# Optimization experiments

Hardware: AMD Instinct MI355X
Metric: run time of the kernel (lower is better)

## Reference

```python
import jax, jax.numpy as jnp
import numpy as np

S = 8          # conv_size == octree branching factor
EMBED = 512    # transformer embed_dim
HEAD = 64      # head_dim
NV = 3         # num_vocab (1=empty, 2=mixed, 3=full; 0=padding)
T2 = 8192      # latent tokens T''
LEN1 = T2 * S          # penultimate-layer tokens (65536)
MIX = LEN1 // 4        # number of mixed tokens in penultimate layer
LEN0 = MIX * S         # last-layer tokens (131072)


def _gelu(x):
    return jax.nn.gelu(x, approximate=False)  # torch nn.GELU default (erf)


def _block_conv(x, W, b):
    # BlockConvolution: within each non-overlapping block of S tokens, output
    # offset j has its own kernel over block inputs 0..j (block-causal).
    # x: [T, Cin], W: [S(offset j), Cout, Cin, S(tap i)], b: [S, Cout]
    xb = x.reshape(-1, S, x.shape[-1])                      # [K, S, Cin]
    Wm = W * jnp.tril(jnp.ones((S, S), W.dtype))[:, None, None, :]
    out = jnp.einsum('kic,joci->kjo', xb, Wm) + b[None]
    return out.reshape(-1, W.shape[1])


def _conv(x, W, b):
    # Conv1d kernel=stride=S. x: [T, Cin], W: [Cout, Cin, S] -> [T//S, Cout]
    xb = x.reshape(-1, S, x.shape[-1])
    return jnp.einsum('kic,oci->ko', xb, W) + b


def _deconv(x, W, b):
    # ConvTranspose1d kernel=stride=S. x: [T, Cin], W: [Cin, Cout, S] -> [T*S, Cout]
    out = jnp.einsum('kc,coj->kjo', x, W) + b
    return out.reshape(-1, W.shape[1])


def _pw(x, W, b):
    # pointwise Conv1d(k=1) / nn.Linear. W: [Cout, Cin]
    return x @ W.T + b


def _forward(value, x, emb_table, Wdc, bdc, bc0a_W, bc0a_b, bc0b_W, bc0b_b,
             bc1a_W, bc1a_b, bc1b_W, bc1b_b, Wd1, bd1, Wp1, bp1,
             Wd0, bd0, Wp0, bp0, Wl1, bl1, Wl2, bl2):
    v = value[0]
    val_1 = v[:LEN1]          # penultimate layer values
    val_0 = v[-LEN0:]         # last layer values (depth == max_depth)
    emb_0 = emb_table[val_0]                               # [LEN0, H]
    down = _conv(emb_0, Wdc, bdc)                          # down_convolution -> [MIX, H]
    idx = jnp.nonzero(val_1 == 2, size=MIX, fill_value=0)[0]  # mixed-token positions
    emb_1 = jnp.zeros((LEN1, HEAD), x.dtype).at[idx].set(down)
    # convolution_0: BC, GELU, BC   (applied to emb_0[:, :mix_1*8] == full emb_0)
    e0 = _block_conv(emb_0, bc0a_W, bc0a_b)
    e0 = _block_conv(_gelu(e0), bc0b_W, bc0b_b)
    # convolution_1: GELU, BC, GELU, BC
    e1 = _block_conv(_gelu(emb_1), bc1a_W, bc1a_b)
    e1 = _block_conv(_gelu(e1), bc1b_W, bc1b_b)
    # deconvolution_1: GELU, Deconv(E->H, S), GELU, Conv(k=1)
    y1 = _deconv(_gelu(x[0]), Wd1, bd1)                    # [LEN1, H]
    y1 = _pw(_gelu(y1), Wp1, bp1) + e1
    x0 = y1[idx]                                           # gather mixed rows -> [MIX, H]
    # deconvolution_0: GELU, Deconv(H->H, 8), GELU, Conv(k=1)
    y0 = _deconv(_gelu(x0), Wd0, bd0)                      # [LEN0, H]
    y0 = _pw(_gelu(y0), Wp0, bp0) + e0
    # linear: GELU, Linear(H,H), GELU, Linear(H, num_vocab)
    return _pw(_gelu(_pw(_gelu(y0), Wl1, bl1)), Wl2, bl2)[None]  # [1, LEN0, NV]


def setup_inputs():
    key = jax.random.key(0)
    ks = jax.random.split(key, 28)
    p = lambda k, sh: jax.random.normal(k, sh, jnp.float32) * 0.02
    # penultimate layer: values in {1,3}, every 4th token is mixed (==2)
    v1 = 1 + 2 * jax.random.bernoulli(ks[0], 0.5, (LEN1,)).astype(jnp.int32)
    v1 = v1.at[::4].set(2)
    v0 = jax.random.randint(ks[1], (LEN0,), 1, NV + 1, dtype=jnp.int32)
    value = jnp.concatenate([v1, v0])[None]
    depth = jnp.concatenate([jnp.full((LEN1,), 5, jnp.int32),
                             jnp.full((LEN0,), 6, jnp.int32)])[None]
    pos = jax.random.randint(ks[2], (1, LEN1 + LEN0, 3), 0, 64, dtype=jnp.int32)
    return dict(
        x=jax.random.normal(ks[3], (1, T2, EMBED), jnp.float32),
        value=value, depth=depth, pos=pos,
        emb_table=p(ks[4], (NV + 1, HEAD)).at[0].set(0.0),  # padding_idx=0
        Wdc=p(ks[5], (HEAD, HEAD, S)), bdc=p(ks[6], (HEAD,)),
        bc0a_W=p(ks[7], (S, HEAD, HEAD, S)), bc0a_b=p(ks[8], (S, HEAD)),
        bc0b_W=p(ks[9], (S, HEAD, HEAD, S)), bc0b_b=p(ks[10], (S, HEAD)),
        bc1a_W=p(ks[11], (S, HEAD, HEAD, S)), bc1a_b=p(ks[12], (S, HEAD)),
        bc1b_W=p(ks[13], (S, HEAD, HEAD, S)), bc1b_b=p(ks[14], (S, HEAD)),
        Wd1=p(ks[15], (EMBED, HEAD, S)), bd1=p(ks[16], (HEAD,)),
        Wp1=p(ks[17], (HEAD, HEAD)), bp1=p(ks[18], (HEAD,)),
        Wd0=p(ks[19], (HEAD, HEAD, S)), bd0=p(ks[20], (HEAD,)),
        Wp0=p(ks[21], (HEAD, HEAD)), bp0=p(ks[22], (HEAD,)),
        Wl1=p(ks[23], (HEAD, HEAD)), bl1=p(ks[24], (HEAD,)),
        Wl2=p(ks[25], (NV, HEAD)), bl2=p(ks[26], (NV,)),
    )


def reference(x, value, depth, pos, emb_table, Wdc, bdc, bc0a_W, bc0a_b, bc0b_W, bc0b_b,
              bc1a_W, bc1a_b, bc1b_W, bc1b_b, Wd1, bd1, Wp1, bp1, Wd0, bd0, Wp0, bp0,
              Wl1, bl1, Wl2, bl2):
    del depth, pos  # only used for length bookkeeping in the original; spatial_encoding is None
    return _forward(value, x, emb_table, Wdc, bdc, bc0a_W, bc0a_b, bc0b_W, bc0b_b,
                    bc1a_W, bc1a_b, bc1b_W, bc1b_b, Wd1, bd1, Wp1, bp1,
                    Wd0, bd0, Wp0, bp0, Wl1, bl1, Wl2, bl2)
```

## Files before the change

kernel.cpp:

```cpp
#include <hip/hip_runtime.h>
#include <hip/hip_bf16.h>
#include <cstddef>
#include <cstdint>

#define LEN1 65536
#define MIX  16384
#define LEN0 131072

typedef __hip_bfloat16 bf16;
typedef __attribute__((ext_vector_type(8))) short bfrag;
typedef __attribute__((ext_vector_type(4))) float ffrag;

__device__ __forceinline__ float gelu(float x){
    return 0.5f * x * (1.0f + erff(x * 0.70710678118654752440f));
}
__device__ __forceinline__ unsigned short f2bf_bits(float f){
    bf16 h = __float2bfloat16(f);
    return __builtin_bit_cast(unsigned short, h);
}
__device__ __forceinline__ float bfbits2f(unsigned short u){
    union { unsigned int i; float f; } v; v.i = ((unsigned int)u) << 16; return v.f;
}

__device__ __forceinline__ void gld_lds16(const void* g, void* l){
    __builtin_amdgcn_global_load_lds(
        (const __attribute__((address_space(1))) unsigned int*)g,
        (__attribute__((address_space(3))) unsigned int*)l, 16, 0, 0);
}


__global__ void k_zero4(float4* p){
    p[(size_t)blockIdx.x * 256 + threadIdx.x] = make_float4(0.f, 0.f, 0.f, 0.f);
}

__global__ void k_gelu_bf(const float4* __restrict__ in, ushort* __restrict__ out){
    size_t t = (size_t)blockIdx.x * 256 + threadIdx.x;
    float4 v = in[t];
    ushort4 o;
    o.x = f2bf_bits(gelu(v.x)); o.y = f2bf_bits(gelu(v.y));
    o.z = f2bf_bits(gelu(v.z)); o.w = f2bf_bits(gelu(v.w));
    *reinterpret_cast<ushort4*>(out + 4*t) = o;
}


__global__ void k_count(const int* __restrict__ val1, int* __restrict__ bcount){
    __shared__ int cnt;
    if (threadIdx.x == 0) cnt = 0;
    __syncthreads();
    int p = blockIdx.x * 256 + threadIdx.x;
    int m = (val1[p] == 2) ? 1 : 0;
    unsigned long long b = __ballot(m);
    if ((threadIdx.x & 63) == 0) atomicAdd(&cnt, __popcll(b));
    __syncthreads();
    if (threadIdx.x == 0) bcount[blockIdx.x] = cnt;
}

__global__ void k_scan(const int* __restrict__ bcount, int* __restrict__ bscan){
    __shared__ int s[256];
    int t = threadIdx.x;
    s[t] = bcount[t];
    __syncthreads();
    for (int off = 1; off < 256; off <<= 1){
        int v = (t >= off) ? s[t - off] : 0;
        __syncthreads();
        s[t] += v;
        __syncthreads();
    }
    bscan[t] = s[t] - bcount[t];
}

__global__ void k_write_idx(const int* __restrict__ val1, const int* __restrict__ bscan,
                            int* __restrict__ idx){
    __shared__ int loc[256];
    int t = threadIdx.x;
    int p = blockIdx.x * 256 + t;
    int m = (val1[p] == 2) ? 1 : 0;
    loc[t] = m;
    __syncthreads();
    for (int off = 1; off < 256; off <<= 1){
        int v = (t >= off) ? loc[t - off] : 0;
        __syncthreads();
        loc[t] += v;
        __syncthreads();
    }
    if (m){
        int g = bscan[blockIdx.x] + loc[t] - 1;
        if (g < MIX) idx[g] = p;
    }
}


__global__ void k_prep_PQ(const float* __restrict__ table, const float* __restrict__ Wdc,
                          const float* __restrict__ W0a, float* __restrict__ P,
                          float* __restrict__ Q){
    int tid = blockIdx.x * 256 + threadIdx.x;
    if (tid < 2048){
        int v = tid >> 9, i = (tid >> 6) & 7, o = tid & 63;
        float s = 0.f;
        for (int c = 0; c < 64; ++c) s += table[v*64 + c] * Wdc[(o*64 + c)*8 + i];
        P[tid] = s;
    } else if (tid < 2048 + 16384){
        int e = tid - 2048;
        int v = e >> 12, j = (e >> 9) & 7, i = (e >> 6) & 7, o = e & 63;
        float s = 0.f;
        for (int c = 0; c < 64; ++c) s += table[v*64 + c] * W0a[((j*64 + o)*64 + c)*8 + i];
        Q[e] = s;
    }
}

__global__ void k_prep_W(const float* __restrict__ W0b, const float* __restrict__ W1a,
                         const float* __restrict__ W1b, const float* __restrict__ Wd1,
                         const float* __restrict__ Wd0, const float* __restrict__ Wp1,
                         const float* __restrict__ Wp0, const float* __restrict__ Wl1,
                         ushort* __restrict__ BT0b, ushort* __restrict__ BT1a,
                         ushort* __restrict__ BT1b, ushort* __restrict__ BTd1,
                         ushort* __restrict__ BTd0, ushort* __restrict__ Wp1bf,
                         ushort* __restrict__ Wp0bf, ushort* __restrict__ Wl1p){
    int e = blockIdx.x * 256 + threadIdx.x;
    if (e < 786432){
        int m = e / 262144, r = e % 262144;
        int n = r >> 9, kk = r & 511;
        int j = n >> 6, o = n & 63;
        int i = kk >> 6, c = kk & 63;
        const float* W = (m == 0) ? W0b : ((m == 1) ? W1a : W1b);
        float v = (i <= j) ? W[((j*64 + o)*64 + c)*8 + i] : 0.0f;
        ((m == 0) ? BT0b : ((m == 1) ? BT1a : BT1b))[r] = f2bf_bits(v);
    } else if (e < 1048576){
        int r = e - 786432;
        int n = r >> 9, kk = r & 511;
        int j = n >> 6, o = n & 63;
        BTd1[r] = f2bf_bits(Wd1[(kk*64 + o)*8 + j]);
    } else if (e < 1081344){
        int r = e - 1048576;
        int n = r >> 6, c = r & 63;
        int j = n >> 6, o = n & 63;
        BTd0[r] = f2bf_bits(Wd0[(c*64 + o)*8 + j]);
    } else if (e < 1085440){
        int r = e - 1081344; Wp1bf[r] = f2bf_bits(Wp1[r]);
    } else if (e < 1089536){
        int r = e - 1085440; Wp0bf[r] = f2bf_bits(Wp0[r]);
    } else if (e < 1093632){
        int r = e - 1089536;
        int o2 = r >> 6, kcol = r & 63;
        int kf = kcol >> 5, q = (kcol >> 3) & 3, ee = kcol & 7;
        int o = kf*32 + ((ee < 4) ? (4*q + ee) : (16 + 4*q + ee - 4));
        Wl1p[r] = f2bf_bits(Wl1[o2*64 + o]);
    }
}


__global__ void k_down_scatter(const int* __restrict__ val0, const float* __restrict__ P,
                               const float* __restrict__ bdc, const int* __restrict__ idx,
                               ushort* __restrict__ gemb1){
    int t = blockIdx.x * 256 + threadIdx.x;
    int k = t >> 6, o = t & 63;
    float s = bdc[o];
    #pragma unroll
    for (int i = 0; i < 8; ++i){
        int v = val0[k*8 + i];
        s += P[(v*8 + i)*64 + o];
    }
    gemb1[(size_t)idx[k]*64 + o] = f2bf_bits(gelu(s));
}

__global__ void k_e0a(const int* __restrict__ val0, const float* __restrict__ Q,
                      const float* __restrict__ b0a, ushort* __restrict__ ge0a){
    int t = blockIdx.x * 256 + threadIdx.x;
    int k = t >> 6, o = t & 63;
    int v[8];
    #pragma unroll
    for (int i = 0; i < 8; ++i) v[i] = val0[k*8 + i];
    float acc[8];
    #pragma unroll
    for (int j = 0; j < 8; ++j) acc[j] = b0a[j*64 + o];
    #pragma unroll
    for (int i = 0; i < 8; ++i){
        const float* Qi = Q + v[i]*4096 + i*64 + o;
        #pragma unroll
        for (int j = i; j < 8; ++j) acc[j] += Qi[j*512];
    }
    #pragma unroll
    for (int j = 0; j < 8; ++j)
        ge0a[(size_t)k*512 + j*64 + o] = f2bf_bits(gelu(acc[j]));
}

template<int BM, int GATHER>
__device__ __forceinline__ void gemm_body(
    const ushort* __restrict__ A, const ushort* __restrict__ BT,
    const float* __restrict__ bias, int bmask,
    ushort* __restrict__ out, int N, int K, const int* __restrict__ idxmap,
    int gelu_flag, ushort* Atile, ushort* Btile, int rowBase, int colBase){
    constexpr int MI = BM / 32;
    const int tid  = threadIdx.x;
    const int lane = tid & 63;
    const int wv   = tid >> 6;
    const int wm   = wv >> 1, wn = wv & 1;

    ffrag acc[MI][4];
    #pragma unroll
    for (int mi = 0; mi < MI; ++mi)
        #pragma unroll
        for (int ni = 0; ni < 4; ++ni)
            #pragma unroll
            for (int r = 0; r < 4; ++r) acc[mi][ni][r] = 0.f;

    constexpr int ACH = BM * 4 / 256;
    int ar[ACH]; int as[ACH]; size_t arow[ACH];
    #pragma unroll
    for (int q = 0; q < ACH; ++q){
        int c = q*256 + tid;
        ar[q] = c >> 2; as[q] = (c & 3) ^ ((ar[q] >> 1) & 3);
        arow[q] = GATHER ? (size_t)idxmap[rowBase + ar[q]] : (size_t)(rowBase + ar[q]);
    }
    int b0c = tid, b1c = 256 + tid;
    int br0 = b0c >> 2, bs0 = (b0c & 3) ^ ((br0 >> 1) & 3);
    int br1 = b1c >> 2, bs1 = (b1c & 3) ^ ((br1 >> 1) & 3);

    for (int kt = 0; kt < K; kt += 32){
        #pragma unroll
        for (int q = 0; q < ACH; ++q)
            gld_lds16(A + arow[q]*K + kt + as[q]*8, (char*)Atile + (q*256 + tid)*16);
        gld_lds16(BT + (size_t)(colBase + br0)*K + kt + bs0*8, (char*)Btile + b0c*16);
        gld_lds16(BT + (size_t)(colBase + br1)*K + kt + bs1*8, (char*)Btile + b1c*16);
        __syncthreads();
        bfrag af[MI], bf[4];
        #pragma unroll
        for (int mi = 0; mi < MI; ++mi){
            int r = wm*(BM/2) + mi*16 + (lane & 15);
            int slot = (lane >> 4) ^ ((r >> 1) & 3);
            af[mi] = *reinterpret_cast<const bfrag*>((const char*)Atile + r*64 + slot*16);
        }
        #pragma unroll
        for (int ni = 0; ni < 4; ++ni){
            int r = wn*64 + ni*16 + (lane & 15);
            int slot = (lane >> 4) ^ ((r >> 1) & 3);
            bf[ni] = *reinterpret_cast<const bfrag*>((const char*)Btile + r*64 + slot*16);
        }
        #pragma unroll
        for (int mi = 0; mi < MI; ++mi)
            #pragma unroll
            for (int ni = 0; ni < 4; ++ni)
                acc[mi][ni] = __builtin_amdgcn_mfma_f32_16x16x32_bf16(af[mi], bf[ni], acc[mi][ni], 0, 0, 0);
        __syncthreads();
    }

    #pragma unroll
    for (int mi = 0; mi < MI; ++mi){
        #pragma unroll
        for (int ni = 0; ni < 4; ++ni){
            int col = colBase + wn*64 + ni*16 + (lane & 15);
            float bv = bias[col & bmask];
            #pragma unroll
            for (int r = 0; r < 4; ++r){
                size_t row = (size_t)rowBase + wm*(BM/2) + mi*16 + (lane >> 4)*4 + r;
                float v = acc[mi][ni][r] + bv;
                if (gelu_flag) v = gelu(v);
                out[row*N + col] = f2bf_bits(v);
            }
        }
    }
}

template<int BM, int GATHER>
__global__ __launch_bounds__(256) void k_mfma_gemm(
    const ushort* __restrict__ A, const ushort* __restrict__ BT,
    const float* __restrict__ bias, int bmask,
    ushort* __restrict__ out, int N, int K, const int* __restrict__ idxmap,
    int gelu_flag){
    __shared__ ushort Atile[BM*32];
    __shared__ ushort Btile[128*32];
    gemm_body<BM, GATHER>(A, BT, bias, bmask, out, N, K, idxmap, gelu_flag,
                          Atile, Btile, blockIdx.y * BM, blockIdx.x * 128);
}

__global__ __launch_bounds__(256) void k_gemm3(
    const ushort* __restrict__ A0, const ushort* __restrict__ A1, const ushort* __restrict__ A2,
    const ushort* __restrict__ B0, const ushort* __restrict__ B1, const ushort* __restrict__ B2,
    const float* __restrict__ bias0, const float* __restrict__ bias1, const float* __restrict__ bias2,
    int bm0, int bm1, int bm2,
    ushort* __restrict__ o0, ushort* __restrict__ o1, ushort* __restrict__ o2,
    int g0, int g1, int g2){
    int b = blockIdx.x;
    int wg = (b & 7) * 128 + (b >> 3);
    const ushort *A, *BT; const float* bias; ushort* out; int bmask, gf, by, bx;
    if (wg < 512){       A = A0; BT = B0; bias = bias0; out = o0; bmask = bm0; gf = g0; by = wg >> 2;        bx = wg & 3; }
    else if (wg < 768){  A = A1; BT = B1; bias = bias1; out = o1; bmask = bm1; gf = g1; by = (wg-512) >> 2;  bx = wg & 3; }
    else {               A = A2; BT = B2; bias = bias2; out = o2; bmask = bm2; gf = g2; by = (wg-768) >> 2;  bx = wg & 3; }
    __shared__ ushort Atile[128*32];
    __shared__ ushort Btile[128*32];
    gemm_body<128, 0>(A, BT, bias, bmask, out, 512, 512, nullptr, gf,
                      Atile, Btile, by * 128, bx * 128);
}

__global__ __launch_bounds__(256) void k_pw(
    const ushort* __restrict__ A, const ushort* __restrict__ W,
    const ushort* __restrict__ res, const float* __restrict__ bias,
    ushort* __restrict__ out){
    __shared__ float bs[64];
    const int tid = threadIdx.x;
    if (tid < 64) bs[tid] = bias[tid];
    const int lane = tid & 63, wv = tid >> 6;
    const int l15 = lane & 15, q = lane >> 4;
    bfrag wf[4][2];
    #pragma unroll
    for (int ni = 0; ni < 4; ++ni)
        #pragma unroll
        for (int kk = 0; kk < 2; ++kk)
            wf[ni][kk] = *reinterpret_cast<const bfrag*>(W + (ni*16 + l15)*64 + kk*32 + q*8);
    __syncthreads();
    size_t rowBase = ((size_t)blockIdx.x * 4 + wv) * 64;
    #pragma unroll
    for (int mi = 0; mi < 4; ++mi){
        size_t r0 = rowBase + mi*16;
        bfrag af[2];
        #pragma unroll
        for (int kk = 0; kk < 2; ++kk)
            af[kk] = *reinterpret_cast<const bfrag*>(A + (r0 + l15)*64 + kk*32 + q*8);
        ffrag acc[4];
        #pragma unroll
        for (int ni = 0; ni < 4; ++ni){
            #pragma unroll
            for (int r = 0; r < 4; ++r) acc[ni][r] = 0.f;
            #pragma unroll
            for (int kk = 0; kk < 2; ++kk)
                acc[ni] = __builtin_amdgcn_mfma_f32_16x16x32_bf16(af[kk], wf[ni][kk], acc[ni], 0, 0, 0);
        }
        #pragma unroll
        for (int ni = 0; ni < 4; ++ni){
            int o = ni*16 + l15;
            float bv = bs[o];
            #pragma unroll
            for (int r = 0; r < 4; ++r){
                size_t t = r0 + q*4 + r;
                float v = acc[ni][r] + bv + bfbits2f(res[t*64 + o]);
                out[t*64 + o] = f2bf_bits(gelu(v));
            }
        }
    }
}

#define TAIL_G 4
__global__ __launch_bounds__(256) void k_tail(
    const ushort* __restrict__ y0dg, const ushort* __restrict__ e0,
    const ushort* __restrict__ Wp0bf, const ushort* __restrict__ Wl1p,
    const float* __restrict__ bp0, const float* __restrict__ bl1,
    const float* __restrict__ Wl2, const float* __restrict__ bl2,
    float* __restrict__ out){
    __shared__ float bp0s[64], bl1s[64], wl2s[192];
    const int tid = threadIdx.x;
    if (tid < 64){ bp0s[tid] = bp0[tid]; bl1s[tid] = bl1[tid]; }
    if (tid < 192) wl2s[tid] = Wl2[tid];
    const int lane = tid & 63, wv = tid >> 6;
    const int l15 = lane & 15, q = lane >> 4;
    bfrag wp0f[4][2], wl1f[4][2];
    #pragma unroll
    for (int of = 0; of < 4; ++of)
        #pragma unroll
        for (int kk = 0; kk < 2; ++kk){
            wp0f[of][kk] = *reinterpret_cast<const bfrag*>(Wp0bf + (of*16 + l15)*64 + kk*32 + q*8);
            wl1f[of][kk] = *reinterpret_cast<const bfrag*>(Wl1p  + (of*16 + l15)*64 + kk*32 + q*8);
        }
    float b20 = bl2[0], b21 = bl2[1], b22 = bl2[2];
    __syncthreads();

    size_t tokBase = ((size_t)blockIdx.x * 4 + wv) * (16 * TAIL_G);
    for (int g = 0; g < TAIL_G; ++g){
        size_t tok0 = tokBase + g*16;
        bfrag yb[2];
        #pragma unroll
        for (int kk = 0; kk < 2; ++kk)
            yb[kk] = *reinterpret_cast<const bfrag*>(y0dg + (tok0 + l15)*64 + kk*32 + q*8);
        ffrag d1[4];
        #pragma unroll
        for (int of = 0; of < 4; ++of){
            #pragma unroll
            for (int r = 0; r < 4; ++r) d1[of][r] = 0.f;
            #pragma unroll
            for (int kk = 0; kk < 2; ++kk)
                d1[of] = __builtin_amdgcn_mfma_f32_16x16x32_bf16(wp0f[of][kk], yb[kk], d1[of], 0, 0, 0);
        }
        float h0[16];
        #pragma unroll
        for (int of = 0; of < 4; ++of)
            #pragma unroll
            for (int r = 0; r < 4; ++r){
                int o = of*16 + q*4 + r;
                float v = d1[of][r] + bp0s[o] + bfbits2f(e0[(tok0 + l15)*64 + o]);
                h0[of*4 + r] = gelu(v);
            }
        bfrag b2[2];
        #pragma unroll
        for (int kf = 0; kf < 2; ++kf)
            #pragma unroll
            for (int e = 0; e < 8; ++e)
                b2[kf][e] = (short)f2bf_bits(h0[(2*kf + (e >> 2))*4 + (e & 3)]);
        ffrag d2[4];
        #pragma unroll
        for (int o2f = 0; o2f < 4; ++o2f){
            #pragma unroll
            for (int r = 0; r < 4; ++r) d2[o2f][r] = 0.f;
            #pragma unroll
            for (int kf = 0; kf < 2; ++kf)
                d2[o2f] = __builtin_amdgcn_mfma_f32_16x16x32_bf16(wl1f[o2f][kf], b2[kf], d2[o2f], 0, 0, 0);
        }
        float s0 = 0.f, s1 = 0.f, s2 = 0.f;
        #pragma unroll
        for (int o2f = 0; o2f < 4; ++o2f)
            #pragma unroll
            for (int r = 0; r < 4; ++r){
                int o2 = o2f*16 + q*4 + r;
                float h1 = gelu(d2[o2f][r] + bl1s[o2]);
                s0 += h1 * wl2s[o2];
                s1 += h1 * wl2s[64 + o2];
                s2 += h1 * wl2s[128 + o2];
            }
        s0 += __shfl_xor(s0, 16); s0 += __shfl_xor(s0, 32);
        s1 += __shfl_xor(s1, 16); s1 += __shfl_xor(s1, 32);
        s2 += __shfl_xor(s2, 16); s2 += __shfl_xor(s2, 32);
        if (q == 0){
            size_t t = tok0 + l15;
            out[t*3 + 0] = s0 + b20;
            out[t*3 + 1] = s1 + b21;
            out[t*3 + 2] = s2 + b22;
        }
    }
}


extern "C" void kernel_launch(void* const* d_in, const int* in_sizes, int n_in,
                              void* d_out, int out_size, void* d_ws, size_t ws_size,
                              hipStream_t stream){
    (void)in_sizes; (void)n_in; (void)out_size; (void)ws_size;
    const float* x     = (const float*)d_in[0];
    const int*   value = (const int*)  d_in[1];
    const float* table = (const float*)d_in[4];
    const float* Wdc   = (const float*)d_in[5];
    const float* bdc   = (const float*)d_in[6];
    const float* W0a   = (const float*)d_in[7];
    const float* b0a   = (const float*)d_in[8];
    const float* W0b   = (const float*)d_in[9];
    const float* b0b   = (const float*)d_in[10];
    const float* W1a   = (const float*)d_in[11];
    const float* b1a   = (const float*)d_in[12];
    const float* W1b   = (const float*)d_in[13];
    const float* b1b   = (const float*)d_in[14];
    const float* Wd1   = (const float*)d_in[15];
    const float* bd1   = (const float*)d_in[16];
    const float* Wp1   = (const float*)d_in[17];
    const float* bp1   = (const float*)d_in[18];
    const float* Wd0   = (const float*)d_in[19];
    const float* bd0   = (const float*)d_in[20];
    const float* Wp0   = (const float*)d_in[21];
    const float* bp0   = (const float*)d_in[22];
    const float* Wl1   = (const float*)d_in[23];
    const float* bl1   = (const float*)d_in[24];
    const float* Wl2   = (const float*)d_in[25];
    const float* bl2   = (const float*)d_in[26];
    float* out = (float*)d_out;

    float* ws = (float*)d_ws;
    size_t off = 0;
    auto alloc = [&](size_t n){ float* p = ws + off; off += (n + 255) & ~(size_t)255; return p; };
    float*  P     = alloc(2048);
    float*  Q     = alloc(16384);
    ushort* BT0b  = (ushort*)alloc(131072);
    ushort* BT1a  = (ushort*)alloc(131072);
    ushort* BT1b  = (ushort*)alloc(131072);
    ushort* BTd1  = (ushort*)alloc(131072);
    ushort* BTd0  = (ushort*)alloc(16384);
    ushort* Wp1bf = (ushort*)alloc(2048);
    ushort* Wp0bf = (ushort*)alloc(2048);
    ushort* Wl1p  = (ushort*)alloc(2048);
    int*    idx    = (int*)alloc(16384);
    int*    bcount = (int*)alloc(256);
    int*    bscan  = (int*)alloc(256);
    ushort* gx_bf    = (ushort*)alloc(2097152);
    ushort* gemb1_bf = (ushort*)alloc(2097152);
    ushort* ge0a_bf  = (ushort*)alloc(4194304);
    ushort* t1_bf    = (ushort*)alloc(2097152);
    ushort* e1_bf    = (ushort*)alloc(2097152);
    ushort* y1g_bf   = (ushort*)alloc(2097152);
    ushort* e0_bf    = (ushort*)alloc(4194304);
    ushort* y1pg_bf  = (ushort*)alloc(2097152);
    ushort* y0dg_bf  = (ushort*)alloc(4194304);

    const int* val1 = value;
    const int* val0 = value + LEN1;

    k_zero4<<<dim3(16), dim3(256), 0, stream>>>((float4*)idx);
    k_count<<<dim3(256), dim3(256), 0, stream>>>(val1, bcount);
    k_scan<<<dim3(1), dim3(256), 0, stream>>>(bcount, bscan);
    k_write_idx<<<dim3(256), dim3(256), 0, stream>>>(val1, bscan, idx);

    k_prep_PQ<<<dim3(72), dim3(256), 0, stream>>>(table, Wdc, W0a, P, Q);
    k_prep_W<<<dim3(4272), dim3(256), 0, stream>>>(W0b, W1a, W1b, Wd1, Wd0, Wp1, Wp0, Wl1,
                                                   BT0b, BT1a, BT1b, BTd1, BTd0, Wp1bf, Wp0bf, Wl1p);

    k_gelu_bf<<<dim3(4096), dim3(256), 0, stream>>>((const float4*)x, gx_bf);

    k_zero4<<<dim3(2048), dim3(256), 0, stream>>>((float4*)gemb1_bf);
    k_down_scatter<<<dim3(4096), dim3(256), 0, stream>>>(val0, P, bdc, idx, gemb1_bf);

    k_e0a<<<dim3(4096), dim3(256), 0, stream>>>(val0, Q, b0a, ge0a_bf);

    k_gemm3<<<dim3(1024), dim3(256), 0, stream>>>(
        ge0a_bf, gemb1_bf, gx_bf,
        BT0b,    BT1a,     BTd1,
        b0b,     b1a,      bd1,
        511,     511,      63,
        e0_bf,   t1_bf,    y1g_bf,
        0,       1,        1);

    k_mfma_gemm<64,0><<<dim3(4,128), dim3(256), 0, stream>>>(t1_bf, BT1b, b1b, 511,
        e1_bf, 512, 512, nullptr, 0);

    k_pw<<<dim3(256), dim3(256), 0, stream>>>(y1g_bf, Wp1bf, e1_bf, bp1, y1pg_bf);

    k_mfma_gemm<64,1><<<dim3(4,256), dim3(256), 0, stream>>>(y1pg_bf, BTd0, bd0, 63,
        y0dg_bf, 512, 64, idx, 1);

    k_tail<<<dim3(512), dim3(256), 0, stream>>>(y0dg_bf, e0_bf, Wp0bf, Wl1p,
                                                bp0, bl1, Wl2, bl2, out);
}
```

Measured before the change: 267.6 us.

## Merge prep kernels, double-buffer GEMM LDS tiles, and widen pw/tail grids

Collapses the many small preprocessing launches (count, scan, index write, PQ prep, weight prep, gelu, zeroing, down-scatter, e0a) into three multi-role kernels to cut launch and serialization overhead. The MFMA GEMM body gets double-buffered LDS tiles with explicit vmcnt waits, so the next K-slice loads while the current one computes. The pointwise and tail kernels process fewer rows per block and launch twice as many blocks for more parallelism. The costs are doubled shared memory per GEMM block, hand-tuned waitcnt values that must match the load count, and a redundant scan in every index block.

```diff
diff --git a/kernel.cpp b/kernel.cpp
--- a/kernel.cpp
+++ b/kernel.cpp
@@ -11,6 +11,8 @@
 typedef __attribute__((ext_vector_type(8))) short bfrag;
 typedef __attribute__((ext_vector_type(4))) float ffrag;
 
+#define VM(n) asm volatile("s_waitcnt vmcnt(" #n ")" ::: "memory")
+
 __device__ __forceinline__ float gelu(float x){
     return 0.5f * x * (1.0f + erff(x * 0.70710678118654752440f));
 }
@@ -28,160 +30,155 @@
         (__attribute__((address_space(3))) unsigned int*)l, 16, 0, 0);
 }
 
-
-__global__ void k_zero4(float4* p){
-    p[(size_t)blockIdx.x * 256 + threadIdx.x] = make_float4(0.f, 0.f, 0.f, 0.f);
-}
-
-__global__ void k_gelu_bf(const float4* __restrict__ in, ushort* __restrict__ out){
-    size_t t = (size_t)blockIdx.x * 256 + threadIdx.x;
-    float4 v = in[t];
-    ushort4 o;
-    o.x = f2bf_bits(gelu(v.x)); o.y = f2bf_bits(gelu(v.y));
-    o.z = f2bf_bits(gelu(v.z)); o.w = f2bf_bits(gelu(v.w));
-    *reinterpret_cast<ushort4*>(out + 4*t) = o;
-}
-
-
-__global__ void k_count(const int* __restrict__ val1, int* __restrict__ bcount){
+__global__ __launch_bounds__(256) void k_L1(
+    const int* __restrict__ val1, int* __restrict__ bcount,
+    const float* __restrict__ table, const float* __restrict__ Wdc,
+    const float* __restrict__ W0a, float* __restrict__ P, float* __restrict__ Q,
+    const float* __restrict__ W0b, const float* __restrict__ W1a,
+    const float* __restrict__ W1b, const float* __restrict__ Wd1,
+    const float* __restrict__ Wd0, const float* __restrict__ Wp1,
+    const float* __restrict__ Wp0, const float* __restrict__ Wl1,
+    ushort* __restrict__ BT0b, ushort* __restrict__ BT1a,
+    ushort* __restrict__ BT1b, ushort* __restrict__ BTd1,
+    ushort* __restrict__ BTd0, ushort* __restrict__ Wp1bf,
+    ushort* __restrict__ Wp0bf, ushort* __restrict__ Wl1p,
+    const float4* __restrict__ x, ushort* __restrict__ gx){
     __shared__ int cnt;
-    if (threadIdx.x == 0) cnt = 0;
-    __syncthreads();
-    int p = blockIdx.x * 256 + threadIdx.x;
-    int m = (val1[p] == 2) ? 1 : 0;
-    unsigned long long b = __ballot(m);
-    if ((threadIdx.x & 63) == 0) atomicAdd(&cnt, __popcll(b));
-    __syncthreads();
-    if (threadIdx.x == 0) bcount[blockIdx.x] = cnt;
-}
-
-__global__ void k_scan(const int* __restrict__ bcount, int* __restrict__ bscan){
-    __shared__ int s[256];
-    int t = threadIdx.x;
-    s[t] = bcount[t];
-    __syncthreads();
-    for (int off = 1; off < 256; off <<= 1){
-        int v = (t >= off) ? s[t - off] : 0;
+    int b = blockIdx.x, tid = threadIdx.x;
+    if (b < 256){
+        if (tid == 0) cnt = 0;
         __syncthreads();
-        s[t] += v;
+        int p = b * 256 + tid;
+        int m = (val1[p] == 2) ? 1 : 0;
+        unsigned long long bl = __ballot(m);
+        if ((tid & 63) == 0) atomicAdd(&cnt, __popcll(bl));
         __syncthreads();
-    }
-    bscan[t] = s[t] - bcount[t];
-}
-
-__global__ void k_write_idx(const int* __restrict__ val1, const int* __restrict__ bscan,
-                            int* __restrict__ idx){
+        if (tid == 0) bcount[b] = cnt;
+    } else if (b < 328){
+        int t = (b - 256) * 256 + tid;
+        if (t < 2048){
+            int v = t >> 9, i = (t >> 6) & 7, o = t & 63;
+            float s = 0.f;
+            for (int c = 0; c < 64; ++c) s += table[v*64 + c] * Wdc[(o*64 + c)*8 + i];
+            P[t] = s;
+        } else {
+            int e = t - 2048;
+            int v = e >> 12, j = (e >> 9) & 7, i = (e >> 6) & 7, o = e & 63;
+            float s = 0.f;
+            for (int c = 0; c < 64; ++c) s += table[v*64 + c] * W0a[((j*64 + o)*64 + c)*8 + i];
+            Q[e] = s;
+        }
+    } else if (b < 4600){
+        int e = (b - 328) * 256 + tid;
+        if (e < 786432){
+            int m = e / 262144, r = e % 262144;
+            int n = r >> 9, kk = r & 511;
+            int j = n >> 6, o = n & 63;
+            int i = kk >> 6, c = kk & 63;
+            const float* W = (m == 0) ? W0b : ((m == 1) ? W1a : W1b);
+            float v = (i <= j) ? W[((j*64 + o)*64 + c)*8 + i] : 0.0f;
+            ((m == 0) ? BT0b : ((m == 1) ? BT1a : BT1b))[r] = f2bf_bits(v);
+        } else if (e < 1048576){
+            int r = e - 786432;
+            int n = r >> 9, kk = r & 511;
+            int j = n >> 6, o = n & 63;
+            BTd1[r] = f2bf_bits(Wd1[(kk*64 + o)*8 + j]);
+        } else if (e < 1081344){
+            int r = e - 1048576;
+            int n = r >> 6, c = r & 63;
+            int j = n >> 6, o = n & 63;
+            BTd0[r] = f2bf_bits(Wd0[(c*64 + o)*8 + j]);
+        } else if (e < 1085440){
+            int r = e - 1081344; Wp1bf[r] = f2bf_bits(Wp1[r]);
+        } else if (e < 1089536){
+            int r = e - 1085440; Wp0bf[r] = f2bf_bits(Wp0[r]);
+        } else {
+            int r = e - 1089536;
+            int o2 = r >> 6, kcol = r & 63;
+            int kf = kcol >> 5, q = (kcol >> 3) & 3, ee = kcol & 7;
+            int o = kf*32 + ((ee < 4) ? (4*q + ee) : (16 + 4*q + ee - 4));
+            Wl1p[r] = f2bf_bits(Wl1[o2*64 + o]);
+        }
+    } else {
+        size_t t = (size_t)(b - 4600) * 256 + tid;
+        float4 v = x[t];
+        ushort4 o;
+        o.x = f2bf_bits(gelu(v.x)); o.y = f2bf_bits(gelu(v.y));
+        o.z = f2bf_bits(gelu(v.z)); o.w = f2bf_bits(gelu(v.w));
+        *reinterpret_cast<ushort4*>(gx + 4*t) = o;
+    }
+}
+
+__global__ __launch_bounds__(256) void k_L2(
+    const int* __restrict__ val1, const int* __restrict__ bcount,
+    int* __restrict__ idx, float4* __restrict__ gemb1z){
+    __shared__ int sb[256];
     __shared__ int loc[256];
-    int t = threadIdx.x;
-    int p = blockIdx.x * 256 + t;
-    int m = (val1[p] == 2) ? 1 : 0;
-    loc[t] = m;
-    __syncthreads();
-    for (int off = 1; off < 256; off <<= 1){
-        int v = (t >= off) ? loc[t - off] : 0;
+    int b = blockIdx.x, t = threadIdx.x;
+    if (b < 256){
+        sb[t] = bcount[t];
         __syncthreads();
-        loc[t] += v;
+        for (int off = 1; off < 256; off <<= 1){
+            int v = (t >= off) ? sb[t - off] : 0;
+            __syncthreads();
+            sb[t] += v;
+            __syncthreads();
+        }
+        int base = (b > 0) ? sb[b - 1] : 0;
+        int p = b * 256 + t;
+        int m = (val1[p] == 2) ? 1 : 0;
+        loc[t] = m;
         __syncthreads();
-    }
-    if (m){
-        int g = bscan[blockIdx.x] + loc[t] - 1;
-        if (g < MIX) idx[g] = p;
-    }
-}
-
-
-__global__ void k_prep_PQ(const float* __restrict__ table, const float* __restrict__ Wdc,
-                          const float* __restrict__ W0a, float* __restrict__ P,
-                          float* __restrict__ Q){
-    int tid = blockIdx.x * 256 + threadIdx.x;
-    if (tid < 2048){
-        int v = tid >> 9, i = (tid >> 6) & 7, o = tid & 63;
-        float s = 0.f;
-        for (int c = 0; c < 64; ++c) s += table[v*64 + c] * Wdc[(o*64 + c)*8 + i];
-        P[tid] = s;
-    } else if (tid < 2048 + 16384){
-        int e = tid - 2048;
-        int v = e >> 12, j = (e >> 9) & 7, i = (e >> 6) & 7, o = e & 63;
-        float s = 0.f;
-        for (int c = 0; c < 64; ++c) s += table[v*64 + c] * W0a[((j*64 + o)*64 + c)*8 + i];
-        Q[e] = s;
-    }
-}
-
-__global__ void k_prep_W(const float* __restrict__ W0b, const float* __restrict__ W1a,
-                         const float* __restrict__ W1b, const float* __restrict__ Wd1,
-                         const float* __restrict__ Wd0, const float* __restrict__ Wp1,
-                         const float* __restrict__ Wp0, const float* __restrict__ Wl1,
-                         ushort* __restrict__ BT0b, ushort* __restrict__ BT1a,
-                         ushort* __restrict__ BT1b, ushort* __restrict__ BTd1,
-                         ushort* __restrict__ BTd0, ushort* __restrict__ Wp1bf,
-                         ushort* __restrict__ Wp0bf, ushort* __restrict__ Wl1p){
-    int e = blockIdx.x * 256 + threadIdx.x;
-    if (e < 786432){
-        int m = e / 262144, r = e % 262144;
-        int n = r >> 9, kk = r & 511;
-        int j = n >> 6, o = n & 63;
-        int i = kk >> 6, c = kk & 63;
-        const float* W = (m == 0) ? W0b : ((m == 1) ? W1a : W1b);
-        float v = (i <= j) ? W[((j*64 + o)*64 + c)*8 + i] : 0.0f;
-        ((m == 0) ? BT0b : ((m == 1) ? BT1a : BT1b))[r] = f2bf_bits(v);
-    } else if (e < 1048576){
-        int r = e - 786432;
-        int n = r >> 9, kk = r & 511;
-        int j = n >> 6, o = n & 63;
-        BTd1[r] = f2bf_bits(Wd1[(kk*64 + o)*8 + j]);
-    } else if (e < 1081344){
-        int r = e - 1048576;
-        int n = r >> 6, c = r & 63;
-        int j = n >> 6, o = n & 63;
-        BTd0[r] = f2bf_bits(Wd0[(c*64 + o)*8 + j]);
-    } else if (e < 1085440){
-        int r = e - 1081344; Wp1bf[r] = f2bf_bits(Wp1[r]);
-    } else if (e < 1089536){
-        int r = e - 1085440; Wp0bf[r] = f2bf_bits(Wp0[r]);
-    } else if (e < 1093632){
-        int r = e - 1089536;
-        int o2 = r >> 6, kcol = r & 63;
-        int kf = kcol >> 5, q = (kcol >> 3) & 3, ee = kcol & 7;
-        int o = kf*32 + ((ee < 4) ? (4*q + ee) : (16 + 4*q + ee - 4));
-        Wl1p[r] = f2bf_bits(Wl1[o2*64 + o]);
-    }
-}
-
-
-__global__ void k_down_scatter(const int* __restrict__ val0, const float* __restrict__ P,
-                               const float* __restrict__ bdc, const int* __restrict__ idx,
-                               ushort* __restrict__ gemb1){
-    int t = blockIdx.x * 256 + threadIdx.x;
-    int k = t >> 6, o = t & 63;
-    float s = bdc[o];
-    #pragma unroll
-    for (int i = 0; i < 8; ++i){
-        int v = val0[k*8 + i];
-        s += P[(v*8 + i)*64 + o];
-    }
-    gemb1[(size_t)idx[k]*64 + o] = f2bf_bits(gelu(s));
-}
-
-__global__ void k_e0a(const int* __restrict__ val0, const float* __restrict__ Q,
-                      const float* __restrict__ b0a, ushort* __restrict__ ge0a){
-    int t = blockIdx.x * 256 + threadIdx.x;
-    int k = t >> 6, o = t & 63;
-    int v[8];
-    #pragma unroll
-    for (int i = 0; i < 8; ++i) v[i] = val0[k*8 + i];
-    float acc[8];
-    #pragma unroll
-    for (int j = 0; j < 8; ++j) acc[j] = b0a[j*64 + o];
-    #pragma unroll
-    for (int i = 0; i < 8; ++i){
-        const float* Qi = Q + v[i]*4096 + i*64 + o;
-        #pragma unroll
-        for (int j = i; j < 8; ++j) acc[j] += Qi[j*512];
-    }
-    #pragma unroll
-    for (int j = 0; j < 8; ++j)
-        ge0a[(size_t)k*512 + j*64 + o] = f2bf_bits(gelu(acc[j]));
+        for (int off = 1; off < 256; off <<= 1){
+            int v = (t >= off) ? loc[t - off] : 0;
+            __syncthreads();
+            loc[t] += v;
+            __syncthreads();
+        }
+        if (m){
+            int g = base + loc[t] - 1;
+            if (g < MIX) idx[g] = p;
+        }
+    } else {
+        gemb1z[(size_t)(b - 256) * 256 + t] = make_float4(0.f, 0.f, 0.f, 0.f);
+    }
+}
+
+__global__ __launch_bounds__(256) void k_L3(
+    const int* __restrict__ val0, const float* __restrict__ P,
+    const float* __restrict__ Q, const float* __restrict__ bdc,
+    const float* __restrict__ b0a, const int* __restrict__ idx,
+    ushort* __restrict__ gemb1, ushort* __restrict__ ge0a){
+    int b = blockIdx.x, tid = threadIdx.x;
+    if (b < 4096){
+        int t = b * 256 + tid;
+        int k = t >> 6, o = t & 63;
+        float s = bdc[o];
+        #pragma unroll
+        for (int i = 0; i < 8; ++i){
+            int v = val0[k*8 + i];
+            s += P[(v*8 + i)*64 + o];
+        }
+        gemb1[(size_t)idx[k]*64 + o] = f2bf_bits(gelu(s));
+    } else {
+        int t = (b - 4096) * 256 + tid;
+        int k = t >> 6, o = t & 63;
+        int v[8];
+        #pragma unroll
+        for (int i = 0; i < 8; ++i) v[i] = val0[k*8 + i];
+        float acc[8];
+        #pragma unroll
+        for (int j = 0; j < 8; ++j) acc[j] = b0a[j*64 + o];
+        #pragma unroll
+        for (int i = 0; i < 8; ++i){
+            const float* Qi = Q + v[i]*4096 + i*64 + o;
+            #pragma unroll
+            for (int j = i; j < 8; ++j) acc[j] += Qi[j*512];
+        }
+        #pragma unroll
+        for (int j = 0; j < 8; ++j)
+            ge0a[(size_t)k*512 + j*64 + o] = f2bf_bits(gelu(acc[j]));
+    }
 }
 
 template<int BM, int GATHER>
@@ -191,6 +188,7 @@
     ushort* __restrict__ out, int N, int K, const int* __restrict__ idxmap,
     int gelu_flag, ushort* Atile, ushort* Btile, int rowBase, int colBase){
     constexpr int MI = BM / 32;
+    constexpr int ACH = BM * 4 / 256;
     const int tid  = threadIdx.x;
     const int lane = tid & 63;
     const int wv   = tid >> 6;
@@ -204,44 +202,63 @@
             #pragma unroll
             for (int r = 0; r < 4; ++r) acc[mi][ni][r] = 0.f;
 
-    constexpr int ACH = BM * 4 / 256;
-    int ar[ACH]; int as[ACH]; size_t arow[ACH];
+    int as_[ACH]; size_t arow[ACH];
     #pragma unroll
     for (int q = 0; q < ACH; ++q){
         int c = q*256 + tid;
-        ar[q] = c >> 2; as[q] = (c & 3) ^ ((ar[q] >> 1) & 3);
-        arow[q] = GATHER ? (size_t)idxmap[rowBase + ar[q]] : (size_t)(rowBase + ar[q]);
-    }
-    int b0c = tid, b1c = 256 + tid;
-    int br0 = b0c >> 2, bs0 = (b0c & 3) ^ ((br0 >> 1) & 3);
-    int br1 = b1c >> 2, bs1 = (b1c & 3) ^ ((br1 >> 1) & 3);
-
-    for (int kt = 0; kt < K; kt += 32){
+        int r = c >> 2; as_[q] = (c & 3) ^ ((r >> 1) & 3);
+        arow[q] = GATHER ? (size_t)idxmap[rowBase + r] : (size_t)(rowBase + r);
+    }
+    const int b0c = tid, b1c = 256 + tid;
+    const int br0 = b0c >> 2, bs0 = (b0c & 3) ^ ((br0 >> 1) & 3);
+    const int br1 = b1c >> 2, bs1 = (b1c & 3) ^ ((br1 >> 1) & 3);
+
+    const int nst = K >> 5;
+    auto stage = [&](int t, int bsel){
+        const int kt = t * 32;
+        char* Ab = (char*)Atile + bsel * (BM * 64);
+        char* Bb = (char*)Btile + bsel * (128 * 64);
         #pragma unroll
         for (int q = 0; q < ACH; ++q)
-            gld_lds16(A + arow[q]*K + kt + as[q]*8, (char*)Atile + (q*256 + tid)*16);
-        gld_lds16(BT + (size_t)(colBase + br0)*K + kt + bs0*8, (char*)Btile + b0c*16);
-        gld_lds16(BT + (size_t)(colBase + br1)*K + kt + bs1*8, (char*)Btile + b1c*16);
-        __syncthreads();
+            gld_lds16(A + arow[q]*K + kt + as_[q]*8, Ab + (q*256 + tid)*16);
+        gld_lds16(BT + (size_t)(colBase + br0)*K + kt + bs0*8, Bb + b0c*16);
+        gld_lds16(BT + (size_t)(colBase + br1)*K + kt + bs1*8, Bb + b1c*16);
+    };
+
+    stage(0, 0);
+    int buf = 0;
+    for (int t = 0; t < nst; ++t){
+        if (t + 1 < nst){
+            stage(t + 1, buf ^ 1);
+            if constexpr (ACH == 2) VM(4); else VM(3);
+        } else {
+            VM(0);
+        }
+        __builtin_amdgcn_s_barrier();
+        __builtin_amdgcn_sched_barrier(0);
+        const char* Ab = (const char*)Atile + buf * (BM * 64);
+        const char* Bb = (const char*)Btile + buf * (128 * 64);
         bfrag af[MI], bf[4];
         #pragma unroll
         for (int mi = 0; mi < MI; ++mi){
             int r = wm*(BM/2) + mi*16 + (lane & 15);
             int slot = (lane >> 4) ^ ((r >> 1) & 3);
-            af[mi] = *reinterpret_cast<const bfrag*>((const char*)Atile + r*64 + slot*16);
+            af[mi] = *reinterpret_cast<const bfrag*>(Ab + r*64 + slot*16);
         }
         #pragma unroll
         for (int ni = 0; ni < 4; ++ni){
             int r = wn*64 + ni*16 + (lane & 15);
             int slot = (lane >> 4) ^ ((r >> 1) & 3);
-            bf[ni] = *reinterpret_cast<const bfrag*>((const char*)Btile + r*64 + slot*16);
+            bf[ni] = *reinterpret_cast<const bfrag*>(Bb + r*64 + slot*16);
         }
         #pragma unroll
         for (int mi = 0; mi < MI; ++mi)
             #pragma unroll
             for (int ni = 0; ni < 4; ++ni)
                 acc[mi][ni] = __builtin_amdgcn_mfma_f32_16x16x32_bf16(af[mi], bf[ni], acc[mi][ni], 0, 0, 0);
-        __syncthreads();
+        __builtin_amdgcn_sched_barrier(0);
+        __builtin_amdgcn_s_barrier();
+        buf ^= 1;
     }
 
     #pragma unroll
@@ -267,8 +284,8 @@
     const float* __restrict__ bias, int bmask,
     ushort* __restrict__ out, int N, int K, const int* __restrict__ idxmap,
     int gelu_flag){
-    __shared__ ushort Atile[BM*32];
-    __shared__ ushort Btile[128*32];
+    __shared__ ushort Atile[2*BM*32];
+    __shared__ ushort Btile[2*128*32];
     gemm_body<BM, GATHER>(A, BT, bias, bmask, out, N, K, idxmap, gelu_flag,
                           Atile, Btile, blockIdx.y * BM, blockIdx.x * 128);
 }
@@ -286,8 +303,8 @@
     if (wg < 512){       A = A0; BT = B0; bias = bias0; out = o0; bmask = bm0; gf = g0; by = wg >> 2;        bx = wg & 3; }
     else if (wg < 768){  A = A1; BT = B1; bias = bias1; out = o1; bmask = bm1; gf = g1; by = (wg-512) >> 2;  bx = wg & 3; }
     else {               A = A2; BT = B2; bias = bias2; out = o2; bmask = bm2; gf = g2; by = (wg-768) >> 2;  bx = wg & 3; }
-    __shared__ ushort Atile[128*32];
-    __shared__ ushort Btile[128*32];
+    __shared__ ushort Atile[2*128*32];
+    __shared__ ushort Btile[2*128*32];
     gemm_body<128, 0>(A, BT, bias, bmask, out, 512, 512, nullptr, gf,
                       Atile, Btile, by * 128, bx * 128);
 }
@@ -308,9 +325,9 @@
         for (int kk = 0; kk < 2; ++kk)
             wf[ni][kk] = *reinterpret_cast<const bfrag*>(W + (ni*16 + l15)*64 + kk*32 + q*8);
     __syncthreads();
-    size_t rowBase = ((size_t)blockIdx.x * 4 + wv) * 64;
+    size_t rowBase = ((size_t)blockIdx.x * 4 + wv) * 32;
     #pragma unroll
-    for (int mi = 0; mi < 4; ++mi){
+    for (int mi = 0; mi < 2; ++mi){
         size_t r0 = rowBase + mi*16;
         bfrag af[2];
         #pragma unroll
@@ -339,7 +356,7 @@
     }
 }
 
-#define TAIL_G 4
+#define TAIL_G 2
 __global__ __launch_bounds__(256) void k_tail(
     const ushort* __restrict__ y0dg, const ushort* __restrict__ e0,
     const ushort* __restrict__ Wp0bf, const ushort* __restrict__ Wl1p,
@@ -473,7 +490,6 @@
     ushort* Wl1p  = (ushort*)alloc(2048);
     int*    idx    = (int*)alloc(16384);
     int*    bcount = (int*)alloc(256);
-    int*    bscan  = (int*)alloc(256);
     ushort* gx_bf    = (ushort*)alloc(2097152);
     ushort* gemb1_bf = (ushort*)alloc(2097152);
     ushort* ge0a_bf  = (ushort*)alloc(4194304);
@@ -487,21 +503,15 @@
     const int* val1 = value;
     const int* val0 = value + LEN1;
 
-    k_zero4<<<dim3(16), dim3(256), 0, stream>>>((float4*)idx);
-    k_count<<<dim3(256), dim3(256), 0, stream>>>(val1, bcount);
-    k_scan<<<dim3(1), dim3(256), 0, stream>>>(bcount, bscan);
-    k_write_idx<<<dim3(256), dim3(256), 0, stream>>>(val1, bscan, idx);
-
-    k_prep_PQ<<<dim3(72), dim3(256), 0, stream>>>(table, Wdc, W0a, P, Q);
-    k_prep_W<<<dim3(4272), dim3(256), 0, stream>>>(W0b, W1a, W1b, Wd1, Wd0, Wp1, Wp0, Wl1,
-                                                   BT0b, BT1a, BT1b, BTd1, BTd0, Wp1bf, Wp0bf, Wl1p);
-
-    k_gelu_bf<<<dim3(4096), dim3(256), 0, stream>>>((const float4*)x, gx_bf);
-
-    k_zero4<<<dim3(2048), dim3(256), 0, stream>>>((float4*)gemb1_bf);
-    k_down_scatter<<<dim3(4096), dim3(256), 0, stream>>>(val0, P, bdc, idx, gemb1_bf);
-
-    k_e0a<<<dim3(4096), dim3(256), 0, stream>>>(val0, Q, b0a, ge0a_bf);
+    k_L1<<<dim3(8696), dim3(256), 0, stream>>>(
+        val1, bcount, table, Wdc, W0a, P, Q,
+        W0b, W1a, W1b, Wd1, Wd0, Wp1, Wp0, Wl1,
+        BT0b, BT1a, BT1b, BTd1, BTd0, Wp1bf, Wp0bf, Wl1p,
+        (const float4*)x, gx_bf);
+
+    k_L2<<<dim3(2304), dim3(256), 0, stream>>>(val1, bcount, idx, (float4*)gemb1_bf);
+
+    k_L3<<<dim3(8192), dim3(256), 0, stream>>>(val0, P, Q, bdc, b0a, idx, gemb1_bf, ge0a_bf);
 
     k_gemm3<<<dim3(1024), dim3(256), 0, stream>>>(
         ge0a_bf, gemb1_bf, gx_bf,
@@ -514,11 +524,11 @@
     k_mfma_gemm<64,0><<<dim3(4,128), dim3(256), 0, stream>>>(t1_bf, BT1b, b1b, 511,
         e1_bf, 512, 512, nullptr, 0);
 
-    k_pw<<<dim3(256), dim3(256), 0, stream>>>(y1g_bf, Wp1bf, e1_bf, bp1, y1pg_bf);
+    k_pw<<<dim3(512), dim3(256), 0, stream>>>(y1g_bf, Wp1bf, e1_bf, bp1, y1pg_bf);
 
     k_mfma_gemm<64,1><<<dim3(4,256), dim3(256), 0, stream>>>(y1pg_bf, BTd0, bd0, 63,
         y0dg_bf, 512, 64, idx, 1);
 
-    k_tail<<<dim3(512), dim3(256), 0, stream>>>(y0dg_bf, e0_bf, Wp0bf, Wl1p,
-                                                bp0, bl1, Wl2, bl2, out);
-}
+    k_tail<<<dim3(1024), dim3(256), 0, stream>>>(y0dg_bf, e0_bf, Wp0bf, Wl1p,
+                                                 bp0, bl1, Wl2, bl2, out);
+}
```

Measured after the change: 251.4 us. -6.0%, faster.
